# Optimization experiments

Hardware: AMD Instinct MI355X
Metric: run time of the kernel (lower is better)

## Reference

```python
import jax, jax.numpy as jnp
import numpy as np

N = 100_000        # nodes
E = 1_600_000      # edges (avg degree 16)
D = 64             # in_feats == hidden_dim
L = 5              # 2 conv-wo-resnet + 3 resnet layers
G = 64             # graphs in the batch
RES_START = 2      # residual connections start at layer index 2
EPS = 1e-5
SLOPE = 0.01       # leaky_relu default negative slope


def setup_inputs() -> dict:
    key = jax.random.key(0)
    ks = jax.random.split(key, 9)
    s = 1.0 / np.sqrt(D)
    return {
        "x": jax.random.normal(ks[0], (N, D), jnp.float32),
        "edge_index": jax.random.randint(ks[1], (2, E), 0, N, dtype=jnp.int32),
        "batch": jnp.sort(jax.random.randint(ks[2], (N,), 0, G, dtype=jnp.int32)),
        "W_l": (jax.random.normal(ks[3], (L, D, D), jnp.float32) * s),   # neighbor lin
        "W_r": (jax.random.normal(ks[4], (L, D, D), jnp.float32) * s),   # root lin
        "b":   (jax.random.normal(ks[5], (L, D), jnp.float32) * s),
        "gn_w":  jnp.ones((L, D), jnp.float32) + 0.1 * jax.random.normal(ks[6], (L, D), jnp.float32),
        "gn_b":  0.1 * jax.random.normal(ks[7], (L, D), jnp.float32),
        "gn_ms": jnp.ones((L, D), jnp.float32) + 0.1 * jax.random.normal(ks[8], (L, D), jnp.float32),
    }


def _mean_agg(x, src, dst):
    # mean aggregation of x[src] into dst (SAGEConv 'mean' aggr)
    summed = jax.ops.segment_sum(x[src], dst, num_segments=N)           # [N, D]
    deg = jax.ops.segment_sum(jnp.ones((src.shape[0],), x.dtype), dst, num_segments=N)
    return summed / jnp.maximum(deg, 1.0)[:, None]


def _sage_bidir(x, edge_index, Wl, Wr, b):
    src, dst = edge_index[0], edge_index[1]
    root = x @ Wr + b
    out_f = _mean_agg(x, src, dst) @ Wl + root
    out_b = _mean_agg(x, dst, src) @ Wl + root   # flipped edges
    return 0.5 * (out_f + out_b)


def _graph_norm(x, batch, w, bias, mean_scale):
    cnt = jnp.maximum(jax.ops.segment_sum(jnp.ones((N,), x.dtype), batch, num_segments=G), 1.0)
    mean = jax.ops.segment_sum(x, batch, num_segments=G) / cnt[:, None]    # [G, D]
    out = x - mean_scale * mean[batch]
    var = jax.ops.segment_sum(out * out, batch, num_segments=G) / cnt[:, None]
    out = out * jax.lax.rsqrt(var + EPS)[batch]
    return w * out + bias


def reference(x, edge_index, batch, W_l, W_r, b, gn_w, gn_b, gn_ms):
    h = x
    for i in range(L):
        h_new = _sage_bidir(h, edge_index, W_l[i], W_r[i], b[i])
        h_new = _graph_norm(h_new, batch, gn_w[i], gn_b[i], gn_ms[i])
        h_new = jnp.where(h_new >= 0, h_new, SLOPE * h_new)   # leaky_relu
        # dropout is identity in eval mode
        h = h_new if i < RES_START else h + h_new
    cnt = jnp.maximum(jax.ops.segment_sum(jnp.ones((N,), h.dtype), batch, num_segments=G), 1.0)
    return jax.ops.segment_sum(h, batch, num_segments=G) / cnt[:, None]   # global_mean_pool [G, D]
```

## Files before the change

kernel.cpp:

```cpp
#include <hip/hip_runtime.h>

#define DD 64
#define GG 64
#define EPSV 1e-5f
#define SLOPE 0.01f

#define NRM_NPW 16
#define NV_WN 32

#define NRANGE 512
#define RSHIFT 8
#define NPR 256
#define ABLK 512

typedef unsigned short ushort_t;
typedef unsigned int uint_t;
typedef float v2f __attribute__((ext_vector_type(2)));
typedef __attribute__((ext_vector_type(8))) short bf16x8;
typedef __attribute__((ext_vector_type(4))) float f32x4;

__device__ __forceinline__ ushort_t f2bf(float f) {
  uint_t u = __float_as_uint(f);
  uint_t r = (u + 0x7fffu + ((u >> 16) & 1u)) >> 16;
  return (ushort_t)r;
}
__device__ __forceinline__ float bf2f(ushort_t s) { return __uint_as_float(((uint_t)s) << 16); }
__device__ __forceinline__ v2f unpk(uint_t u) {
  v2f r;
  r.x = __uint_as_float(u << 16);
  r.y = __uint_as_float(u & 0xffff0000u);
  return r;
}

__global__ __launch_bounds__(256) void bin_count_kernel(const int* __restrict__ src,
                                                        const int* __restrict__ dst,
                                                        int* __restrict__ hist, int E) {
  __shared__ int cf[NRANGE], cb[NRANGE];
  for (int i=threadIdx.x; i<NRANGE; i+=256) { cf[i]=0; cb[i]=0; }
  __syncthreads();
  int epb = (E + ABLK-1)/ABLK;
  int lo = blockIdx.x*epb, hi = lo+epb; if (hi>E) hi=E;
  for (int e=lo+threadIdx.x; e<hi; e+=256) {
    int d = __builtin_nontemporal_load(&dst[e]);
    int s = __builtin_nontemporal_load(&src[e]);
    atomicAdd(&cf[d>>RSHIFT], 1);
    atomicAdd(&cb[s>>RSHIFT], 1);
  }
  __syncthreads();
  for (int r=threadIdx.x; r<NRANGE; r+=256) {
    hist[(size_t)r*ABLK + blockIdx.x]            = cf[r];
    hist[(size_t)(NRANGE+r)*ABLK + blockIdx.x]   = cb[r];
  }
}

__global__ void block_sum_kernel(const int* __restrict__ v, int* __restrict__ partial, int M) {
  __shared__ int sm[1024];
  int i = blockIdx.x*1024 + threadIdx.x;
  sm[threadIdx.x] = (i<M) ? v[i] : 0;
  __syncthreads();
  for (int s=512; s>0; s>>=1) {
    if (threadIdx.x < s) sm[threadIdx.x] += sm[threadIdx.x+s];
    __syncthreads();
  }
  if (threadIdx.x==0) partial[blockIdx.x] = sm[0];
}

__global__ void scan_partial_kernel(int* __restrict__ partial, int nb) {
  __shared__ int sm[512];
  int t = threadIdx.x;
  int v = (t<nb) ? partial[t] : 0;
  int orig = v;
  sm[t] = v; __syncthreads();
  for (int off=1; off<512; off<<=1) {
    int a = (t>=off) ? sm[t-off] : 0;
    __syncthreads();
    v += a; sm[t] = v;
    __syncthreads();
  }
  if (t<nb) partial[t] = v - orig;
}

__global__ void scan_apply_kernel(const int* __restrict__ v, const int* __restrict__ partial,
                                  int* __restrict__ out, int M) {
  __shared__ int sm[1024];
  int i = blockIdx.x*1024 + threadIdx.x;
  int x = (i<M) ? v[i] : 0;
  int orig = x;
  sm[threadIdx.x] = x; __syncthreads();
  for (int off=1; off<1024; off<<=1) {
    int a = (threadIdx.x>=off) ? sm[threadIdx.x-off] : 0;
    __syncthreads();
    x += a; sm[threadIdx.x] = x;
    __syncthreads();
  }
  if (i<M) out[i] = x - orig + partial[blockIdx.x];
}

__global__ __launch_bounds__(256) void bin_scatter_kernel(const int* __restrict__ src,
                                                          const int* __restrict__ dst,
                                                          const int* __restrict__ offs,
                                                          int* __restrict__ staged, int E) {
  __shared__ int ofF[NRANGE], ofB[NRANGE];
  for (int r=threadIdx.x; r<NRANGE; r+=256) {
    ofF[r] = offs[(size_t)r*ABLK + blockIdx.x];
    ofB[r] = offs[(size_t)(NRANGE+r)*ABLK + blockIdx.x];
  }
  __syncthreads();
  int epb = (E + ABLK-1)/ABLK;
  int lo = blockIdx.x*epb, hi = lo+epb; if (hi>E) hi=E;
  for (int e=lo+threadIdx.x; e<hi; e+=256) {
    int d = __builtin_nontemporal_load(&dst[e]);
    int s = __builtin_nontemporal_load(&src[e]);
    int pf = atomicAdd(&ofF[d>>RSHIFT], 1);
    staged[pf] = (s << 8) | (d & (NPR-1));
    int pb = atomicAdd(&ofB[s>>RSHIFT], 1);
    staged[pb] = (d << 8) | (s & (NPR-1));
  }
}

__global__ __launch_bounds__(256) void range_fill_kernel(const int* __restrict__ staged,
                                                         const int* __restrict__ offs,
                                                         int* __restrict__ rp_f, int* __restrict__ rp_b,
                                                         int* __restrict__ col_f, int* __restrict__ col_b,
                                                         int N, int E) {
  __shared__ int cnt[NPR], noff[NPR], sc[NPR];
  int lr = blockIdx.x;
  int d = lr >> 9, r = lr & (NRANGE-1);
  int start = offs[(size_t)lr*ABLK];
  int end   = (lr+1 < 2*NRANGE) ? offs[(size_t)(lr+1)*ABLK] : 2*E;
  int t = threadIdx.x;
  cnt[t] = 0; __syncthreads();
  for (int k=start+t; k<end; k+=256) {
    atomicAdd(&cnt[staged[k] & (NPR-1)], 1);
  }
  __syncthreads();
  int x = cnt[t]; sc[t] = x; __syncthreads();
  for (int off=1; off<NPR; off<<=1) {
    int a = (t>=off) ? sc[t-off] : 0;
    __syncthreads();
    x += a; sc[t] = x;
    __syncthreads();
  }
  noff[t] = x - cnt[t];
  __syncthreads();
  int base = d ? (start - E) : start;
  int node = (r << RSHIFT) + t;
  int* rp = d ? rp_b : rp_f;
  if (node < N)       rp[node] = base + noff[t];
  else if (node == N) rp[N]    = base + noff[t];
  cnt[t] = 0; __syncthreads();
  int* col = d ? col_b : col_f;
  for (int k=start+t; k<end; k+=256) {
    int rec = staged[k];
    int li = rec & (NPR-1);
    int rank = atomicAdd(&cnt[li], 1);
    col[base + noff[li] + rank] = rec >> 8;
  }
}

__global__ void cnt_kernel(const int* __restrict__ batch, int* __restrict__ cnt, int N) {
  __shared__ int hist[GG];
  if (threadIdx.x < GG) hist[threadIdx.x] = 0;
  __syncthreads();
  int i = blockIdx.x*blockDim.x + threadIdx.x;
  int stride = gridDim.x*blockDim.x;
  for (int n=i; n<N; n+=stride) atomicAdd(&hist[batch[n]], 1);
  __syncthreads();
  if (threadIdx.x < GG) atomicAdd(&cnt[threadIdx.x], hist[threadIdx.x]);
}

__global__ void tobf16_kernel(const float* __restrict__ in, ushort_t* __restrict__ out, int M) {
  int i = blockIdx.x*blockDim.x + threadIdx.x;
  int stride = gridDim.x*blockDim.x;
  for (int k=i; k<M; k+=stride) out[k] = f2bf(in[k]);
}

__global__ void wpack_kernel(const float* __restrict__ Wl, const float* __restrict__ Wr,
                             ushort_t* __restrict__ Wb) {
  int l = blockIdx.x;
  const float* wl = Wl + (size_t)l*4096;
  const float* wr = Wr + (size_t)l*4096;
  ushort_t* out = Wb + (size_t)l*8192;
  for (int idx = threadIdx.x; idx < 8192; idx += 256) {
    int kb = idx >> 9, rem = idx & 511, col = rem >> 3, j = rem & 7;
    int k = kb*8 + j;
    float v = (k < 64) ? wl[(size_t)k*64+col] : wr[(size_t)(k-64)*64+col];
    out[idx] = f2bf(v);
  }
}

__global__ __launch_bounds__(256) void gg_kernel(
    const ushort_t* __restrict__ hb,
    const int* __restrict__ rp_f, const int* __restrict__ col_f,
    const int* __restrict__ rp_b, const int* __restrict__ col_b,
    const ushort_t* __restrict__ Wb, const float* __restrict__ bias,
    const int* __restrict__ batch,
    ushort_t* __restrict__ tb, float* __restrict__ gsum, float* __restrict__ gsq, int N)
{
  __shared__ ushort_t srow[16][72];
  __shared__ float lsum[4][DD];
  __shared__ float lsq[4][DD];
  __shared__ ushort_t tbs[16][DD];

  int wid = threadIdx.x >> 6;
  int lane = threadIdx.x & 63;
  int base = blockIdx.x*16;

  for (int i=threadIdx.x; i<4*DD; i+=256) { (&lsum[0][0])[i]=0.f; (&lsq[0][0])[i]=0.f; }

  {
    int qt = lane >> 4;
    int g  = lane & 15;
    const char* hbb = (const char*)hb;
    uint_t goff = (uint_t)g << 3;

    for (int nn=0; nn<4; ++nn) {
      int w = base + wid*4 + nn;
      v2f a01={0.f,0.f}, a23={0.f,0.f}, c01={0.f,0.f}, c23={0.f,0.f};
      int degf=0, degb=0;
      if (w < N) {
        {
          int s0 = rp_f[w], e0 = rp_f[w+1];
          degf = e0 - s0;
          for (int bse=s0; bse<e0; bse+=64) {
            int m = e0-bse; if (m>64) m=64;
            int jv = (lane<m) ? col_f[bse+lane] : 0;
            int q=0;
            for (; 4*q+16 <= m; q+=4) {
              int j0=__shfl(jv,4*q+qt),    j1=__shfl(jv,4*q+4+qt);
              int j2=__shfl(jv,4*q+8+qt),  j3=__shfl(jv,4*q+12+qt);
              uint2 v0 = *(const uint2*)(hbb + ((((uint_t)j0)<<7) | goff));
              uint2 v1 = *(const uint2*)(hbb + ((((uint_t)j1)<<7) | goff));
              uint2 v2 = *(const uint2*)(hbb + ((((uint_t)j2)<<7) | goff));
              uint2 v3 = *(const uint2*)(hbb + ((((uint_t)j3)<<7) | goff));
              a01 += unpk(v0.x); a23 += unpk(v0.y);
              a01 += unpk(v1.x); a23 += unpk(v1.y);
              a01 += unpk(v2.x); a23 += unpk(v2.y);
              a01 += unpk(v3.x); a23 += unpk(v3.y);
            }
            for (; 4*q+qt < m; ++q) {
              int j=__shfl(jv,4*q+qt);
              uint2 v = *(const uint2*)(hbb + ((((uint_t)j)<<7) | goff));
              a01 += unpk(v.x); a23 += unpk(v.y);
            }
          }
        }
        {
          int s1 = rp_b[w], e1 = rp_b[w+1];
          degb = e1 - s1;
          for (int bse=s1; bse<e1; bse+=64) {
            int m = e1-bse; if (m>64) m=64;
            int jv = (lane<m) ? col_b[bse+lane] : 0;
            int q=0;
            for (; 4*q+16 <= m; q+=4) {
              int j0=__shfl(jv,4*q+qt),    j1=__shfl(jv,4*q+4+qt);
              int j2=__shfl(jv,4*q+8+qt),  j3=__shfl(jv,4*q+12+qt);
              uint2 v0 = *(const uint2*)(hbb + ((((uint_t)j0)<<7) | goff));
              uint2 v1 = *(const uint2*)(hbb + ((((uint_t)j1)<<7) | goff));
              uint2 v2 = *(const uint2*)(hbb + ((((uint_t)j2)<<7) | goff));
              uint2 v3 = *(const uint2*)(hbb + ((((uint_t)j3)<<7) | goff));
              c01 += unpk(v0.x); c23 += unpk(v0.y);
              c01 += unpk(v1.x); c23 += unpk(v1.y);
              c01 += unpk(v2.x); c23 += unpk(v2.y);
              c01 += unpk(v3.x); c23 += unpk(v3.y);
            }
            for (; 4*q+qt < m; ++q) {
              int j=__shfl(jv,4*q+qt);
              uint2 v = *(const uint2*)(hbb + ((((uint_t)j)<<7) | goff));
              c01 += unpk(v.x); c23 += unpk(v.y);
            }
          }
        }
      }
      float df = fmaxf((float)degf, 1.f);
      float db = fmaxf((float)degb, 1.f);
      float s0v = 0.5f*(a01.x/df + c01.x/db);
      float s1v = 0.5f*(a01.y/df + c01.y/db);
      float s2v = 0.5f*(a23.x/df + c23.x/db);
      float s3v = 0.5f*(a23.y/df + c23.y/db);
      s0v += __shfl_xor(s0v,16); s0v += __shfl_xor(s0v,32);
      s1v += __shfl_xor(s1v,16); s1v += __shfl_xor(s1v,32);
      s2v += __shfl_xor(s2v,16); s2v += __shfl_xor(s2v,32);
      s3v += __shfl_xor(s3v,16); s3v += __shfl_xor(s3v,32);
      if (qt==0) {
        uint2 pk;
        pk.x = (uint_t)f2bf(s0v) | ((uint_t)f2bf(s1v) << 16);
        pk.y = (uint_t)f2bf(s2v) | ((uint_t)f2bf(s3v) << 16);
        *(uint2*)&srow[wid*4+nn][4*g] = pk;
      }
    }
  }
  __syncthreads();

  int lrow = lane & 15;
  int lk   = lane >> 4;

  const ushort_t* sr = &srow[lrow][0];
  bf16x8 a0 = *(const bf16x8*)&sr[lk*8];
  bf16x8 a1 = *(const bf16x8*)&sr[32+lk*8];
  int arow = base + lrow; if (arow >= N) arow = N-1;
  const bf16x8* hfrag = (const bf16x8*)(hb + (size_t)arow*DD);
  bf16x8 a2 = hfrag[lk];
  bf16x8 a3 = hfrag[4+lk];

  const bf16x8* wbp = (const bf16x8*)Wb;
  int col = wid*16 + lrow;
  f32x4 acc = (f32x4){0.f,0.f,0.f,0.f};
  acc = __builtin_amdgcn_mfma_f32_16x16x32_bf16(a0, wbp[(0*4+lk)*64 + col], acc, 0,0,0);
  acc = __builtin_amdgcn_mfma_f32_16x16x32_bf16(a1, wbp[(1*4+lk)*64 + col], acc, 0,0,0);
  acc = __builtin_amdgcn_mfma_f32_16x16x32_bf16(a2, wbp[(2*4+lk)*64 + col], acc, 0,0,0);
  acc = __builtin_amdgcn_mfma_f32_16x16x32_bf16(a3, wbp[(3*4+lk)*64 + col], acc, 0,0,0);

  int g0 = batch[(base < N) ? base : (N-1)];
  int bt[4];
  #pragma unroll
  for (int r=0; r<4; ++r) {
    int node = base + lk*4 + r;
    bt[r] = (node < N) ? batch[node] : -1;
  }
  {
    int feat = wid*16 + lrow;
    float bv = bias[feat];
    int gcur = -1; float ga=0.f, qa=0.f;
    #pragma unroll
    for (int r=0; r<4; ++r) {
      if (bt[r] < 0) break;
      float v = acc[r] + bv;
      tbs[lk*4+r][feat] = f2bf(v);
      if (bt[r] != gcur) {
        if (gcur >= 0) {
          int slot = gcur - g0;
          if (slot < 4) { atomicAdd(&lsum[slot][feat], ga); atomicAdd(&lsq[slot][feat], qa); }
          else { atomicAdd(&gsum[gcur*DD+feat], ga); atomicAdd(&gsq[gcur*DD+feat], qa); }
        }
        gcur = bt[r]; ga = 0.f; qa = 0.f;
      }
      ga += v; qa += v*v;
    }
    if (gcur >= 0) {
      int slot = gcur - g0;
      if (slot < 4) { atomicAdd(&lsum[slot][feat], ga); atomicAdd(&lsq[slot][feat], qa); }
      else { atomicAdd(&gsum[gcur*DD+feat], ga); atomicAdd(&gsq[gcur*DD+feat], qa); }
    }
  }
  __syncthreads();

  int lastnode = base+15; if (lastnode >= N) lastnode = N-1;
  int nslots = batch[lastnode] - g0 + 1; if (nslots > 4) nslots = 4;
  for (int idx=threadIdx.x; idx < nslots*DD; idx += 256) {
    int s = idx >> 6, f = idx & 63;
    float vs = lsum[s][f], vq = lsq[s][f];
    if (vs != 0.f || vq != 0.f) {
      atomicAdd(&gsum[(g0+s)*DD+f], vs);
      atomicAdd(&gsq[(g0+s)*DD+f], vq);
    }
  }
  for (int c=threadIdx.x; c<128; c+=256) {
    int row = c >> 3, off = (c & 7)*8;
    int node = base + row;
    if (node < N) *(bf16x8*)&tb[(size_t)node*DD + off] = *(const bf16x8*)&tbs[row][off];
  }
}

__global__ __launch_bounds__(256) void norm2v_kernel(
    const ushort_t* __restrict__ tb,
    const float* __restrict__ gsum, const float* __restrict__ gsq,
    const int* __restrict__ cnt, const int* __restrict__ batch,
    const float* __restrict__ gw, const float* __restrict__ gb,
    const float* __restrict__ gms,
    ushort_t* __restrict__ hb, int resid, int N)
{
  int wv_id = (blockIdx.x*blockDim.x + threadIdx.x) >> 6;
  int lane = threadIdx.x & 63;
  int oct = lane & 7;
  int no  = lane >> 3;
  int base = wv_id * NV_WN;
  if (base >= N) return;
  float wvv[8], bvv[8], msv[8];
  #pragma unroll
  for (int j=0;j<8;++j){ int f=oct*8+j; wvv[j]=gw[f]; bvv[j]=gb[f]; msv[j]=gms[f]; }
  int gcur=-1; float mean[8], rs[8];
  int end = base + NV_WN; if (end > N) end = N;
  for (int nb=base+no; nb<end; nb+=8) {
    int g = batch[nb];
    if (g != gcur) {
      float invc = 1.f/fmaxf((float)cnt[g],1.f);
      #pragma unroll
      for (int j=0;j<8;++j){
        int f = oct*8+j;
        float mn = gsum[g*DD+f]*invc;
        float mq = gsq[g*DD+f]*invc;
        float var = mq - msv[j]*(2.f-msv[j])*mn*mn;
        mean[j]=mn; rs[j]=rsqrtf(var+EPSV);
      }
      gcur=g;
    }
    bf16x8 tv = *(const bf16x8*)&tb[(size_t)nb*DD + oct*8];
    bf16x8 hv8 = *(const bf16x8*)&hb[(size_t)nb*DD + oct*8];
    bf16x8 outv;
    #pragma unroll
    for (int j=0;j<8;++j){
      float u = bf2f((ushort_t)tv[j]) - msv[j]*mean[j];
      float y = wvv[j]*u*rs[j] + bvv[j];
      y = (y>=0.f) ? y : SLOPE*y;
      float hvv = resid ? (bf2f((ushort_t)hv8[j]) + y) : y;
      outv[j] = (short)f2bf(hvv);
    }
    *(bf16x8*)&hb[(size_t)nb*DD + oct*8] = outv;
  }
}

__global__ void norm2_last_kernel(const ushort_t* __restrict__ tb,
                             const float* __restrict__ gsum, const float* __restrict__ gsq,
                             const int* __restrict__ cnt, const int* __restrict__ batch,
                             const float* __restrict__ gw, const float* __restrict__ gb,
                             const float* __restrict__ gms,
                             const ushort_t* __restrict__ hb,
                             float* __restrict__ pout, int N)
{
  int wid = (blockIdx.x*blockDim.x + threadIdx.x) >> 6;
  int lane = threadIdx.x & 63;
  int base = wid*NRM_NPW;
  if (base >= N) return;
  float wv = gw[lane], bv = gb[lane], msv = gms[lane];
  float cms = msv*(2.f - msv);
  int gcur=-1; float rs=0.f, mean=0.f, pacc=0.f;
  int end = base+NRM_NPW; if (end>N) end=N;
  for (int node=base; node<end; ++node) {
    int g = batch[node];
    if (g!=gcur) {
      if (gcur>=0) atomicAdd(&pout[gcur*DD+lane], pacc);
      pacc = 0.f;
      float invc = 1.f/fmaxf((float)cnt[g],1.f);
      mean = gsum[g*DD+lane]*invc;
      float msq = gsq[g*DD+lane]*invc;
      float var = msq - cms*mean*mean;
      rs = rsqrtf(var + EPSV);
      gcur=g;
    }
    float u = bf2f(tb[(size_t)node*DD+lane]) - msv*mean;
    float y = wv*u*rs + bv;
    y = (y>=0.f) ? y : SLOPE*y;
    pacc += bf2f(hb[(size_t)node*DD+lane]) + y;
  }
  if (gcur>=0) atomicAdd(&pout[gcur*DD+lane], pacc);
}

__global__ void finalize_kernel(const float* __restrict__ pout, const int* __restrict__ cnt,
                                float* __restrict__ out)
{
  int i = blockIdx.x*blockDim.x + threadIdx.x;
  if (i < GG*DD) {
    float invc = 1.f/fmaxf((float)cnt[i>>6],1.f);
    out[i] = pout[i]*invc;
  }
}

extern "C" void kernel_launch(void* const* d_in, const int* in_sizes, int n_in,
                              void* d_out, int out_size, void* d_ws, size_t ws_size,
                              hipStream_t stream)
{
  const float* x    = (const float*)d_in[0];
  const int*  ei    = (const int*)d_in[1];
  const int*  batch = (const int*)d_in[2];
  const float* W_l  = (const float*)d_in[3];
  const float* W_r  = (const float*)d_in[4];
  const float* bias = (const float*)d_in[5];
  const float* gn_w = (const float*)d_in[6];
  const float* gn_b = (const float*)d_in[7];
  const float* gn_ms= (const float*)d_in[8];

  int N = in_sizes[2];
  int E = in_sizes[1]/2;
  int L = in_sizes[5]/DD;
  const int* src = ei;
  const int* dst = ei + E;

  char* p = (char*)d_ws;
  int*   cnt   = (int*)p;   p += GG*4;
  float* gsum  = (float*)p; p += (size_t)L*GG*DD*4;
  float* gsq   = (float*)p; p += (size_t)L*GG*DD*4;
  float* pout  = (float*)p; p += GG*DD*4;
  size_t zeroBytes = (char*)p - (char*)d_ws;

  int* staged  = (int*)p; p += (size_t)2*E*4;
  ushort_t* tb    = (ushort_t*)p; p += (size_t)N*DD*2;
  ushort_t* hb    = (ushort_t*)p; p += (size_t)N*DD*2;
  ushort_t* wb    = (ushort_t*)p; p += (size_t)L*8192*2;
  int* rp_f    = (int*)p; p += (size_t)(N+1)*4;
  int* rp_b    = (int*)p; p += (size_t)(N+1)*4;
  int* col_f   = (int*)p; p += (size_t)E*4;
  int* col_b   = (int*)p; p += (size_t)E*4;
  int* hist    = (int*)p; p += (size_t)2*NRANGE*ABLK*4;
  int* offs    = (int*)p; p += (size_t)2*NRANGE*ABLK*4;
  int* partial = (int*)p; p += 512*4;

  hipMemsetAsync(d_ws, 0, zeroBytes, stream);

  const int M = 2*NRANGE*ABLK;
  bin_count_kernel<<<ABLK, 256, 0, stream>>>(src, dst, hist, E);
  block_sum_kernel<<<(M+1023)/1024, 1024, 0, stream>>>(hist, partial, M);
  scan_partial_kernel<<<1, 512, 0, stream>>>(partial, (M+1023)/1024);
  scan_apply_kernel<<<(M+1023)/1024, 1024, 0, stream>>>(hist, partial, offs, M);
  bin_scatter_kernel<<<ABLK, 256, 0, stream>>>(src, dst, offs, staged, E);
  range_fill_kernel<<<2*NRANGE, 256, 0, stream>>>(staged, offs, rp_f, rp_b, col_f, col_b, N, E);

  cnt_kernel<<<391, 256, 0, stream>>>(batch, cnt, N);
  tobf16_kernel<<<2048, 256, 0, stream>>>(x, hb, N*DD);
  wpack_kernel<<<L, 256, 0, stream>>>(W_l, W_r, wb);

  int ggBlocks = (N + 15)/16;
  int nvWaves = (N + NV_WN-1)/NV_WN;
  int nvBlocks = (nvWaves+3)/4;
  int nrmWaves = (N + NRM_NPW-1)/NRM_NPW;
  int nrmBlocks = (nrmWaves+3)/4;

  for (int i=0; i<L; ++i) {
    float* gsum_i = gsum + (size_t)i*GG*DD;
    float* gsq_i  = gsq  + (size_t)i*GG*DD;
    gg_kernel<<<ggBlocks, 256, 0, stream>>>(hb, rp_f, col_f, rp_b, col_b,
                                            wb + (size_t)i*8192, bias+(size_t)i*DD,
                                            batch, tb, gsum_i, gsq_i, N);
    if (i < L-1) {
      norm2v_kernel<<<nvBlocks, 256, 0, stream>>>(tb, gsum_i, gsq_i, cnt, batch,
                                                  gn_w+(size_t)i*DD, gn_b+(size_t)i*DD,
                                                  gn_ms+(size_t)i*DD, hb, (i>=2)?1:0, N);
    } else {
      norm2_last_kernel<<<nrmBlocks, 256, 0, stream>>>(tb, gsum_i, gsq_i, cnt, batch,
                                                       gn_w+(size_t)i*DD, gn_b+(size_t)i*DD,
                                                       gn_ms+(size_t)i*DD, hb, pout, N);
    }
  }
  finalize_kernel<<<16, 256, 0, stream>>>(pout, cnt, (float*)d_out);
}
```

Measured before the change: 647.8 us.

## Make each wave own 16 nodes end-to-end and drop mid-kernel block barrier

```diff
diff --git a/kernel.cpp b/kernel.cpp
--- a/kernel.cpp
+++ b/kernel.cpp
@@ -197,16 +197,17 @@
     const int* __restrict__ batch,
     ushort_t* __restrict__ tb, float* __restrict__ gsum, float* __restrict__ gsq, int N)
 {
-  __shared__ ushort_t srow[16][72];
-  __shared__ float lsum[4][DD];
-  __shared__ float lsq[4][DD];
-  __shared__ ushort_t tbs[16][DD];
+  __shared__ ushort_t srow[64][72];
+  __shared__ float lsum[8][DD];
+  __shared__ float lsq[8][DD];
 
   int wid = threadIdx.x >> 6;
   int lane = threadIdx.x & 63;
-  int base = blockIdx.x*16;
-
-  for (int i=threadIdx.x; i<4*DD; i+=256) { (&lsum[0][0])[i]=0.f; (&lsq[0][0])[i]=0.f; }
+  int base = blockIdx.x*64;
+  int wbase = base + wid*16;
+
+  for (int i=threadIdx.x; i<8*DD; i+=256) { (&lsum[0][0])[i]=0.f; (&lsq[0][0])[i]=0.f; }
+  __syncthreads();
 
   {
     int qt = lane >> 4;
@@ -214,8 +215,8 @@
     const char* hbb = (const char*)hb;
     uint_t goff = (uint_t)g << 3;
 
-    for (int nn=0; nn<4; ++nn) {
-      int w = base + wid*4 + nn;
+    for (int nn=0; nn<16; ++nn) {
+      int w = wbase + nn;
       v2f a01={0.f,0.f}, a23={0.f,0.f}, c01={0.f,0.f}, c23={0.f,0.f};
       int degf=0, degb=0;
       if (w < N) {
@@ -286,51 +287,56 @@
         uint2 pk;
         pk.x = (uint_t)f2bf(s0v) | ((uint_t)f2bf(s1v) << 16);
         pk.y = (uint_t)f2bf(s2v) | ((uint_t)f2bf(s3v) << 16);
-        *(uint2*)&srow[wid*4+nn][4*g] = pk;
+        *(uint2*)&srow[wid*16+nn][4*g] = pk;
       }
     }
   }
-  __syncthreads();
 
   int lrow = lane & 15;
   int lk   = lane >> 4;
 
-  const ushort_t* sr = &srow[lrow][0];
+  const ushort_t* sr = &srow[wid*16 + lrow][0];
   bf16x8 a0 = *(const bf16x8*)&sr[lk*8];
   bf16x8 a1 = *(const bf16x8*)&sr[32+lk*8];
-  int arow = base + lrow; if (arow >= N) arow = N-1;
+  int arow = wbase + lrow; if (arow >= N) arow = N-1;
   const bf16x8* hfrag = (const bf16x8*)(hb + (size_t)arow*DD);
   bf16x8 a2 = hfrag[lk];
   bf16x8 a3 = hfrag[4+lk];
 
   const bf16x8* wbp = (const bf16x8*)Wb;
-  int col = wid*16 + lrow;
-  f32x4 acc = (f32x4){0.f,0.f,0.f,0.f};
-  acc = __builtin_amdgcn_mfma_f32_16x16x32_bf16(a0, wbp[(0*4+lk)*64 + col], acc, 0,0,0);
-  acc = __builtin_amdgcn_mfma_f32_16x16x32_bf16(a1, wbp[(1*4+lk)*64 + col], acc, 0,0,0);
-  acc = __builtin_amdgcn_mfma_f32_16x16x32_bf16(a2, wbp[(2*4+lk)*64 + col], acc, 0,0,0);
-  acc = __builtin_amdgcn_mfma_f32_16x16x32_bf16(a3, wbp[(3*4+lk)*64 + col], acc, 0,0,0);
+  f32x4 acc[4];
+  #pragma unroll
+  for (int t=0; t<4; ++t) acc[t] = (f32x4){0.f,0.f,0.f,0.f};
+  #pragma unroll
+  for (int t=0; t<4; ++t) {
+    int col = t*16 + lrow;
+    acc[t] = __builtin_amdgcn_mfma_f32_16x16x32_bf16(a0, wbp[(0*4+lk)*64 + col], acc[t], 0,0,0);
+    acc[t] = __builtin_amdgcn_mfma_f32_16x16x32_bf16(a1, wbp[(1*4+lk)*64 + col], acc[t], 0,0,0);
+    acc[t] = __builtin_amdgcn_mfma_f32_16x16x32_bf16(a2, wbp[(2*4+lk)*64 + col], acc[t], 0,0,0);
+    acc[t] = __builtin_amdgcn_mfma_f32_16x16x32_bf16(a3, wbp[(3*4+lk)*64 + col], acc[t], 0,0,0);
+  }
 
   int g0 = batch[(base < N) ? base : (N-1)];
   int bt[4];
   #pragma unroll
   for (int r=0; r<4; ++r) {
-    int node = base + lk*4 + r;
+    int node = wbase + lk*4 + r;
     bt[r] = (node < N) ? batch[node] : -1;
   }
-  {
-    int feat = wid*16 + lrow;
+  #pragma unroll
+  for (int t=0; t<4; ++t) {
+    int feat = t*16 + lrow;
     float bv = bias[feat];
     int gcur = -1; float ga=0.f, qa=0.f;
     #pragma unroll
     for (int r=0; r<4; ++r) {
       if (bt[r] < 0) break;
-      float v = acc[r] + bv;
-      tbs[lk*4+r][feat] = f2bf(v);
+      float v = acc[t][r] + bv;
+      srow[wid*16 + lk*4 + r][feat] = f2bf(v);
       if (bt[r] != gcur) {
         if (gcur >= 0) {
           int slot = gcur - g0;
-          if (slot < 4) { atomicAdd(&lsum[slot][feat], ga); atomicAdd(&lsq[slot][feat], qa); }
+          if (slot < 8) { atomicAdd(&lsum[slot][feat], ga); atomicAdd(&lsq[slot][feat], qa); }
           else { atomicAdd(&gsum[gcur*DD+feat], ga); atomicAdd(&gsq[gcur*DD+feat], qa); }
         }
         gcur = bt[r]; ga = 0.f; qa = 0.f;
@@ -339,14 +345,20 @@
     }
     if (gcur >= 0) {
       int slot = gcur - g0;
-      if (slot < 4) { atomicAdd(&lsum[slot][feat], ga); atomicAdd(&lsq[slot][feat], qa); }
+      if (slot < 8) { atomicAdd(&lsum[slot][feat], ga); atomicAdd(&lsq[slot][feat], qa); }
       else { atomicAdd(&gsum[gcur*DD+feat], ga); atomicAdd(&gsq[gcur*DD+feat], qa); }
     }
   }
-  __syncthreads();
-
-  int lastnode = base+15; if (lastnode >= N) lastnode = N-1;
-  int nslots = batch[lastnode] - g0 + 1; if (nslots > 4) nslots = 4;
+
+  for (int c=lane; c<128; c+=64) {
+    int row = c >> 3, off = (c & 7)*8;
+    int node = wbase + row;
+    if (node < N) *(bf16x8*)&tb[(size_t)node*DD + off] = *(const bf16x8*)&srow[wid*16+row][off];
+  }
+
+  __syncthreads();
+  int lastnode = base+63; if (lastnode >= N) lastnode = N-1;
+  int nslots = batch[lastnode] - g0 + 1; if (nslots > 8) nslots = 8;
   for (int idx=threadIdx.x; idx < nslots*DD; idx += 256) {
     int s = idx >> 6, f = idx & 63;
     float vs = lsum[s][f], vq = lsq[s][f];
@@ -354,11 +366,6 @@
       atomicAdd(&gsum[(g0+s)*DD+f], vs);
       atomicAdd(&gsq[(g0+s)*DD+f], vq);
     }
-  }
-  for (int c=threadIdx.x; c<128; c+=256) {
-    int row = c >> 3, off = (c & 7)*8;
-    int node = base + row;
-    if (node < N) *(bf16x8*)&tb[(size_t)node*DD + off] = *(const bf16x8*)&tbs[row][off];
   }
 }
 
@@ -509,7 +516,7 @@
   tobf16_kernel<<<2048, 256, 0, stream>>>(x, hb, N*DD);
   wpack_kernel<<<L, 256, 0, stream>>>(W_l, W_r, wb);
 
-  int ggBlocks = (N + 15)/16;
+  int ggBlocks = (N + 63)/64;
   int nvWaves = (N + NV_WN-1)/NV_WN;
   int nvBlocks = (nvWaves+3)/4;
   int nrmWaves = (N + NRM_NPW-1)/NRM_NPW;
```

Result: slower. 884.4 us (+36.5%).
